# Kernel optimization log

Hardware: AMD Instinct MI355X
Metric: run time of the kernel (lower is better)

## Reference

```python
import jax, jax.numpy as jnp
import numpy as np

WIN = 15
BINS = 32
ALPHA = 0.9
LAM1 = 0.5
LAM2 = 0.5


def _tmedian(x, axis):
    # torch-style median: k-th smallest with k=(n-1)//2 (lower middle), keepdims
    n = x.shape[axis]
    s = jnp.sort(x, axis=axis)
    return jnp.take(s, jnp.array([(n - 1) // 2]), axis=axis)


def _box_sum_1d(x, k, axis):
    # sliding-window sum (zero padding) via cumsum / integral image
    p = k // 2
    L = x.shape[axis]
    c = jnp.cumsum(x, axis=axis)
    pad = [(0, 0)] * x.ndim
    pad[axis] = (1, 0)
    c = jnp.pad(c, pad)
    i = jnp.arange(L)
    hi = jnp.clip(i + p + 1, 0, L)
    lo = jnp.clip(i - p, 0, L)
    return jnp.take(c, hi, axis=axis) - jnp.take(c, lo, axis=axis)


def _counts_1d(L, k, dtype):
    p = k // 2
    i = jnp.arange(L)
    return (jnp.clip(i + p + 1, 0, L) - jnp.clip(i - p, 0, L)).astype(dtype)


def box_avg(x, k):
    # avg_pool2d(stride=1, padding=k//2, count_include_pad=False) on [B,C,H,W]
    s = _box_sum_1d(_box_sum_1d(x, k, 2), k, 3)
    c = _counts_1d(x.shape[2], k, x.dtype)[:, None] * _counts_1d(x.shape[3], k, x.dtype)[None, :]
    return s / c


def avg3(x):
    # avg_pool2d(k=3, stride=1, pad=1, count_include_pad=True)
    return _box_sum_1d(_box_sum_1d(x, 3, 2), 3, 3) / 9.0


def _softplus(x):
    t = jnp.log1p(jnp.exp(-jnp.abs(x)))
    return jnp.where(x >= 0, x + t, t)


def _conv3(x, k):
    return jax.lax.conv_general_dilated(x, k, (1, 1), ((1, 1), (1, 1)),
                                        dimension_numbers=('NCHW', 'OIHW', 'NCHW'))


def _forward(lab, a_rand):
    B, _, H, W = lab.shape
    N = H * W
    f32 = lab.dtype
    L = lab[:, 0:1]
    a = lab[:, 1:2]
    b = lab[:, 2:3]
    kx = jnp.array([[-1, 0, 1], [-2, 0, 2], [-1, 0, 1]], f32).reshape(1, 1, 3, 3)
    ky = jnp.array([[-1, -2, -1], [0, 0, 0], [1, 2, 1]], f32).reshape(1, 1, 3, 3)
    gx = _conv3(L, kx)
    gy = _conv3(L, ky)
    E = avg3(gx * gx) + avg3(gy * gy)           # structure-tensor trace
    S = jnp.sqrt(a * a + b * b + 1e-8)           # chroma
    Xf = jnp.concatenate([E, S], 1).reshape(B, 2, N).transpose(0, 2, 1)   # [B,N,2]
    yf = L.reshape(B, 1, N).transpose(0, 2, 1)                            # [B,N,1]
    XtX = jnp.einsum('bni,bnj->bij', Xf, Xf)
    XtY = jnp.einsum('bni,bnj->bij', Xf, yf)
    beta = jnp.linalg.solve(XtX + 1e-6 * jnp.eye(2, dtype=f32), XtY)[..., 0]  # [B,2]
    pred = beta[:, 0][:, None, None, None] * E + beta[:, 1][:, None, None, None] * S
    L_perp = L - pred
    # robust scale + whitening of [L_perp, E, S]
    X3f = jnp.concatenate([L_perp, E, S], 1).reshape(B, 3, N).transpose(0, 2, 1)  # [B,N,3]
    med = _tmedian(X3f, 1)
    mad = _tmedian(jnp.abs(X3f - med), 1) * 1.4826 + 1e-8
    Xz = (X3f - med) / mad
    diff = Xz - Xz.mean(1, keepdims=True)
    cov = jnp.einsum('bni,bnj->bij', diff, diff) / N
    e, V = jnp.linalg.eigh(jnp.maximum(cov, 1e-8))
    Wwh = jnp.einsum('bij,bj,bkj->bik', V, 1.0 / jnp.sqrt(e), V)
    Xw = diff @ Wwh                                                       # [B,N,3]
    # 128-way random-projection kurtosis search
    an = a_rand / (jnp.linalg.norm(a_rand, axis=-1, keepdims=True) + 1e-12)
    z = jnp.einsum('bni,bti->bnt', Xw, an)                                # [B,N,128]
    zc = z - z.mean(1, keepdims=True)
    m2 = (zc ** 2).mean(1) + 1e-12
    m4 = (zc ** 4).mean(1)
    kurt = m4 / (m2 * m2) - 3.0
    best = jnp.argmax(jnp.abs(kurt), axis=1)
    a_star = jnp.take_along_axis(an, best[:, None, None], axis=1)[:, 0]   # [B,3]
    z_best = jnp.einsum('bni,bi->bn', Xw, a_star)                         # [B,N]
    # 1-D 2-component GMM, 10 EM steps
    K = 2
    q25 = jnp.quantile(z_best, 0.25, axis=1)
    q75 = jnp.quantile(z_best, 0.75, axis=1)
    mu = jnp.stack([q25, q75], 1)[:, None, :]   # [B,1,K]
    var = jnp.ones((B, 1, K), f32)
    pi = jnp.full((B, 1, K), 0.5, f32)
    x1 = z_best[:, :, None]                      # [B,N,1]
    R = jnp.zeros((B, N, K), f32)
    for _ in range(10):
        logp = (-0.5 * ((x1 - mu) ** 2 / (var + 1e-6))
                - 0.5 * jnp.log(var + 1e-6) + jnp.log(pi + 1e-8))
        R = jnp.exp(jax.nn.log_softmax(logp, axis=2))
        Nk = R.sum(1, keepdims=True)             # [B,1,K]
        mu = (R * x1).sum(1, keepdims=True) / (Nk + 1e-8)
        var = (R * (x1 - mu) ** 2).sum(1, keepdims=True) / (Nk + 1e-8) + 1e-6
        pi = Nk / N
    R_alpha = R ** ALPHA
    R_alpha = R_alpha / (R_alpha.sum(2, keepdims=True) + 1e-8)
    rk_maps = R_alpha.transpose(0, 2, 1).reshape(B, K, 1, H, W)
    # per-cluster weighted Mahalanobis distance in [L_perp,E,S] space
    eye3 = jnp.eye(3, dtype=f32)
    Dk = []
    for k in range(K):
        w = R_alpha[:, :, k]
        Wsum = w.sum(1, keepdims=True) + 1e-8
        mu_k = jnp.einsum('bn,bni->bi', w, X3f) / Wsum
        Xm = X3f - mu_k[:, None, :]
        cov_k = jnp.einsum('bn,bni,bnj->bij', w, Xm, Xm) / Wsum[..., None] + 1e-6 * eye3
        inv_k = jnp.linalg.inv(cov_k)
        Dk.append(jnp.sqrt(jnp.einsum('bni,bij,bnj->bn', Xm, inv_k, Xm) + 1e-8))
    Dk = jnp.stack(Dk, 2)                        # [B,N,K]
    Rtemp = jax.nn.softmax(jnp.log(R_alpha + 1e-8), axis=2)
    D_M = (Rtemp * Dk).sum(2).reshape(B, 1, H, W)
    # local luminance anomaly (box-filtered weighted mean/std)
    Z_LLA = []
    for k in range(K):
        rk = rk_maps[:, k]
        den = box_avg(rk, WIN) + 1e-8
        mu_b = box_avg(rk * L_perp, WIN) / den
        var_b = jnp.maximum(box_avg(rk * L_perp ** 2, WIN) / den - mu_b ** 2, 1e-8)
        lla = jnp.abs(L_perp - mu_b) / (jnp.sqrt(var_b) + 1e-8)
        v = lla.reshape(B, 1, N)
        mv = _tmedian(v, 2)
        mdv = _tmedian(jnp.abs(v - mv), 2) * 1.4826 + 1e-8
        Z_LLA.append(((v - mv) / mdv).reshape(B, 1, H, W))
    # global-vs-local histogram distance (GLD)
    Lmin = L_perp.min(axis=(2, 3), keepdims=True)
    Lmax = L_perp.max(axis=(2, 3), keepdims=True)
    Lnorm = jnp.clip((L_perp - Lmin) / (Lmax - Lmin + 1e-8), 0, 1)
    idx = jnp.clip((Lnorm * BINS).astype(jnp.int32), 0, BINS - 1)[:, 0]   # [B,H,W]
    onehot = jax.nn.one_hot(idx, BINS, dtype=f32).transpose(0, 3, 1, 2)   # [B,bins,H,W]
    Z_GLD = []
    for k in range(K):
        rk = rk_maps[:, k]
        w_hist = onehot * rk
        g_hist = w_hist.reshape(B, BINS, N).sum(-1)
        g_hist = g_hist / (g_hist.sum(1, keepdims=True) + 1e-8)
        g_cdf = jnp.cumsum(g_hist, 1)
        loc_cdf = jnp.cumsum(box_avg(w_hist, WIN), 1) / (box_avg(rk, WIN) + 1e-8)
        GLD = jnp.abs(loc_cdf - g_cdf[:, :, None, None]).sum(1) / BINS    # [B,H,W]
        v = GLD.reshape(B, N)
        mv = _tmedian(v, 1)                                              # [B,1]
        mdv = _tmedian(jnp.abs(v - mv), 1) * 1.4826 + 1e-8
        Z_GLD.append(((GLD - mv[:, :, None]) / mdv[:, :, None])[:, None])
    gamma = jnp.ones_like(L_perp)
    for k in range(K):
        gamma = gamma + rk_maps[:, k] * (LAM1 * _softplus(Z_LLA[k]) + LAM2 * _softplus(Z_GLD[k]))
    # structural decorrelation term over [E,S]
    ES = jnp.concatenate([E, S], 1).reshape(B, 2, N).transpose(0, 2, 1)
    med2 = _tmedian(ES, 1)
    mad2 = _tmedian(jnp.abs(ES - med2), 1) * 1.4826 + 1e-8
    ESz = (ES - med2) / mad2
    d = ESz - ESz.mean(1, keepdims=True)
    cov2 = jnp.einsum('bni,bnj->bij', d, d) / N + 1e-6 * jnp.eye(2, dtype=f32)
    inv2 = jnp.linalg.inv(cov2)
    d2 = jnp.einsum('bni,bij,bnj->bn', d, inv2, d).reshape(B, 1, H, W)
    R_struct = jnp.exp(-0.5 * d2)
    L_anom = jnp.maximum(D_M * gamma * (1.0 - R_struct), 0.0)
    flat = L_anom.reshape(B, -1)
    q1 = jnp.quantile(flat, 0.01, axis=1).reshape(B, 1, 1, 1)
    q9 = jnp.quantile(flat, 0.99, axis=1).reshape(B, 1, 1, 1)
    L_anom_norm = jnp.clip((L_anom - q1) / (q9 - q1 + 1e-8), 0, 1)
    return L_perp, L_anom_norm


def setup_inputs() -> dict:
    key = jax.random.key(0)
    k1, k2 = jax.random.split(key)
    return {
        'batch_lab_raw': jax.random.normal(k1, (2, 3, 384, 384), jnp.float32),
        'a_rand': jax.random.normal(k2, (2, 128, 3), jnp.float32),
    }


def reference(batch_lab_raw, a_rand):
    return _forward(batch_lab_raw, a_rand)
```

## Files before the change

kernel.cpp:

```cpp
#include <hip/hip_runtime.h>
#include <math.h>

#define HH 384
#define WW 384
#define NPIX (HH*WW)
#define NB 2
#define BN (NB*NPIX)
#define NT 128
#define NBINS 32
#define MEDRANK ((NPIX-1)/2)
#define RB 72
#define RB2 288
#define SEL_BLK 64
#define KDG 8
#define KSEG 16
#define GHS 496
#define GVS 272

#define A_BETA 0
#define A_XZ   16
#define A_ES   40
#define A_DK   56
#define A_GMM  128
#define A_ZTOT 272
#define A_GHIST 288
#define A_KURT 512

#define F_BETA 0
#define F_X3   8
#define F_MEAN 24
#define F_WWH  32
#define F_ASTAR 828
#define F_ZBQ  868
#define F_DKINV 880
#define F_CM   918
#define F_ESI  940
#define F_LAQ  952
#define F_GCDF 968
#define F_MMS_MIN 1280
#define F_MMS_MAX 1408

__device__ __forceinline__ double waveSum(double v){
#pragma unroll
  for(int o=32;o;o>>=1) v += __shfl_down(v,o,64);
  return v;
}
__device__ __forceinline__ unsigned f2u(float f){
  unsigned u = __float_as_uint(f);
  return (u & 0x80000000u) ? ~u : (u | 0x80000000u);
}
__device__ __forceinline__ float u2f(unsigned u){
  return __uint_as_float((u & 0x80000000u) ? (u ^ 0x80000000u) : ~u);
}
__device__ __forceinline__ float sp(float x){
  float t = log1pf(expf(-fabsf(x)));
  return x >= 0.f ? x + t : t;
}

struct SelBatch {
  const float* src[8];
  int rank[8];
  int fslot[8];
  int nt;
  int medmad;
};

__device__ void pickN(const unsigned* hp, int nb, int rank, unsigned& sel, int& nrank){
  __shared__ unsigned s_cum[256];
  __shared__ unsigned s_res[2];
  int tid = threadIdx.x;
  int base = tid*8;
  unsigned loc[8]; unsigned tsum=0;
#pragma unroll
  for(int j=0;j<8;j++){ unsigned v=(base+j<nb)?hp[base+j]:0u; loc[j]=v; tsum+=v; }
  s_cum[tid]=tsum;
  __syncthreads();
  for(int o=1;o<256;o<<=1){
    unsigned t=(tid>=o)?s_cum[tid-o]:0u;
    __syncthreads();
    s_cum[tid]+=t;
    __syncthreads();
  }
  unsigned cum=s_cum[tid], ex=cum-tsum;
  if(tsum>0u && (unsigned)rank>=ex && (unsigned)rank<cum){
    int rr=rank-(int)ex; unsigned bsel=0;
#pragma unroll
    for(int j=0;j<8;j++){ if((unsigned)rr<loc[j]){ bsel=(unsigned)(base+j); break; } rr-=(int)loc[j]; }
    s_res[0]=bsel; s_res[1]=(unsigned)rr;
  }
  __syncthreads();
  sel=s_res[0]; nrank=(int)s_res[1];
  __syncthreads();
}

__global__ void k_zero(double* A, float* F, unsigned* T, unsigned* H){
  int i = blockIdx.x*256 + threadIdx.x;
  if(i < 2048) A[i] = 0.0;
  if(i < 4096){
    unsigned* U = (unsigned*)F;
    unsigned v = 0u;
    if(i>=F_MMS_MIN && i<F_MMS_MIN+64) v = 0xFFFFFFFFu;
    U[i] = v;
  }
  if(i < 512) T[i] = 0u;
  for(int j=i; j<240*2048; j+=65536) H[j]=0u;
}

__global__ __launch_bounds__(256) void k_selp(SelBatch sb, unsigned* Hh, unsigned* T,
                                              float* F, int bid, int stage, int p){
  int task = blockIdx.x / SEL_BLK;
  int blk  = blockIdx.x % SEL_BLK;
  unsigned* meta = T + 384 + task*8;
  float center = (stage==1) ? __uint_as_float(meta[4]) : 0.f;
  unsigned pre = (p==2) ? 0u : meta[stage*2];
  __shared__ unsigned lh[2048];
  for(int j=threadIdx.x;j<2048;j+=256) lh[j]=0u;
  __syncthreads();
  const float* src = sb.src[task];
  for(int i=blk*256+threadIdx.x; i<NPIX; i+=SEL_BLK*256){
    float v = src[i];
    if(stage) v = fabsf(v-center);
    unsigned u = f2u(v);
    unsigned bin; bool ok;
    if(p==2){ bin = u>>21; ok = true; }
    else if(p==1){ bin = (u>>10)&2047u; ok = ((u>>21)==pre); }
    else { bin = u&1023u; ok = ((u>>10)==pre); }
    if(ok) atomicAdd(&lh[bin],1u);
  }
  __syncthreads();
  unsigned* hp = Hh + (size_t)(((bid*8+task)*2+stage)*3 + (2-p))*2048;
  for(int j=threadIdx.x;j<2048;j+=256){ unsigned c=lh[j]; if(c) atomicAdd(hp+j,c); }
  __shared__ int s_last;
  __syncthreads();
  if(threadIdx.x==0){
    __threadfence();
    s_last = (atomicAdd(&T[16+bid*64+task*8+stage*4+(2-p)],1u) == (unsigned)(SEL_BLK-1));
  }
  __syncthreads();
  if(!s_last) return;
  int r = (p==2) ? sb.rank[task] : (int)meta[stage*2+1];
  int nb = (p==0) ? 1024 : 2048;
  unsigned sel; int nr;
  pickN(hp, nb, r, sel, nr);
  if(threadIdx.x==0){
    if(p==2){ meta[stage*2]=sel; meta[stage*2+1]=(unsigned)nr; }
    else if(p==1){ meta[stage*2]=(pre<<11)|sel; meta[stage*2+1]=(unsigned)nr; }
    else {
      float val = u2f((pre<<10)|sel);
      if(stage==0){
        if(sb.medmad) meta[4]=__float_as_uint(val);
        else F[sb.fslot[task]]=val;
      } else {
        F[sb.fslot[task]]   = __uint_as_float(meta[4]);
        F[sb.fslot[task]+1] = val*1.4826f + 1e-8f;
      }
    }
  }
}

__device__ void quad_from_stats(double N0,double Sx0,double Sxx0,double Sxt,double Sxxt,
                                float& qa,float& qb,float& qc){
  double Nt=(double)NPIX;
  double N1=Nt-N0, Sx1=Sxt-Sx0, Sxx1=Sxxt-Sxx0;
  double mu0=Sx0/(N0+1e-8), mu1=Sx1/(N1+1e-8);
  double v0=(Sxx0-2.0*mu0*Sx0+mu0*mu0*N0)/(N0+1e-8)+1e-6;
  double v1=(Sxx1-2.0*mu1*Sx1+mu1*mu1*N1)/(N1+1e-8)+1e-6;
  double p0=N0/Nt, p1=N1/Nt;
  double c0=-0.5*log(v0+1e-6)+log(p0+1e-8);
  double c1=-0.5*log(v1+1e-6)+log(p1+1e-8);
  double iv0=0.5/(v0+1e-6), iv1=0.5/(v1+1e-6);
  qa=(float)(iv0-iv1);
  qb=(float)(2.0*(iv1*mu1-iv0*mu0));
  qc=(float)(iv0*mu0*mu0-iv1*mu1*mu1+c1-c0);
}
__device__ void quad_init(const float* F,int b,float& qa,float& qb,float& qc){
  const float* z = F + F_ZBQ + b*4;
  double h25 = 0.25*(double)(NPIX-1); double f25 = h25 - floor(h25);
  double h75 = 0.75*(double)(NPIX-1); double f75 = h75 - floor(h75);
  double mu0 = (double)z[0] + f25*((double)z[1]-(double)z[0]);
  double mu1 = (double)z[2] + f75*((double)z[3]-(double)z[2]);
  double iv = 0.5/(1.0+1e-6);
  qa = 0.f;
  qb = (float)(2.0*iv*(mu1-mu0));
  qc = (float)(iv*(mu0*mu0-mu1*mu1));
}

__global__ __launch_bounds__(256) void k_sobel(const float* lab, float* S, float* E){
  int bx = blockIdx.x % 24, by = (blockIdx.x/24) % 24, b = blockIdx.x/576;
  __shared__ float Lt[20][21];
  __shared__ float G[18][19];
  const float* Lb = lab + b*3*NPIX;
  int ox = bx*16, oy = by*16;
  for(int i=threadIdx.x; i<400; i+=256){
    int lx=i%20, ly=i/20;
    int gx_=ox-2+lx, gy_=oy-2+ly;
    Lt[ly][lx] = (gx_<0||gx_>=WW||gy_<0||gy_>=HH)?0.f:Lb[gy_*WW+gx_];
  }
  __syncthreads();
  for(int i=threadIdx.x; i<324; i+=256){
    int lx=i%18, ly=i/18;
    int px=lx+1, py=ly+1;
    int gxp=ox-2+px, gyp=oy-2+py;
    float g=0.f;
    if(gxp>=0&&gxp<WW&&gyp>=0&&gyp<HH){
      float gx = -Lt[py-1][px-1]+Lt[py-1][px+1] -2.f*Lt[py][px-1]+2.f*Lt[py][px+1] -Lt[py+1][px-1]+Lt[py+1][px+1];
      float gy = -Lt[py-1][px-1]-2.f*Lt[py-1][px]-Lt[py-1][px+1] +Lt[py+1][px-1]+2.f*Lt[py+1][px]+Lt[py+1][px+1];
      g = gx*gx+gy*gy;
    }
    G[ly][lx]=g;
  }
  __syncthreads();
  int tx = threadIdx.x%16, ty = threadIdx.x/16;
  float s=0;
#pragma unroll
  for(int dy=0;dy<3;dy++)
#pragma unroll
    for(int dx=0;dx<3;dx++) s += G[ty+dy][tx+dx];
  int n = (oy+ty)*WW + ox+tx;
  E[b*NPIX+n] = s*(1.f/9.f);
  float av=Lb[NPIX+n], bv=Lb[2*NPIX+n];
  S[b*NPIX+n] = sqrtf(av*av+bv*bv+1e-8f);
}

__global__ void k_beta_red(const float* E,const float* S,const float* lab,double* A,
                           float* F, unsigned* T){
  int b = blockIdx.x / RB, blk = blockIdx.x % RB;
  double s[5]={0,0,0,0,0};
  for(int n = blk*256 + threadIdx.x; n < NPIX; n += RB*256){
    float e=E[b*NPIX+n], ss=S[b*NPIX+n], l=lab[b*3*NPIX+n];
    s[0]+=(double)e*e; s[1]+=(double)e*ss; s[2]+=(double)ss*ss;
    s[3]+=(double)e*l; s[4]+=(double)ss*l;
  }
  __shared__ double red[4][5];
  int wave=threadIdx.x>>6, lane=threadIdx.x&63;
#pragma unroll
  for(int q=0;q<5;q++){
    s[q]=waveSum(s[q]);
    if(lane==0) red[wave][q]=s[q];
  }
  __syncthreads();
  if(threadIdx.x<5){
    double v = red[0][threadIdx.x]+red[1][threadIdx.x]+red[2][threadIdx.x]+red[3][threadIdx.x];
    atomicAdd(&A[A_BETA+b*5+threadIdx.x], v);
  }
  __shared__ int s_last;
  __syncthreads();
  if(threadIdx.x==0){
    __threadfence();
    s_last = (atomicAdd(&T[0],1u) == (unsigned)(NB*RB-1));
  }
  __syncthreads();
  if(!s_last || threadIdx.x) return;
  for(int bb=0;bb<NB;bb++){
    double EE=A[A_BETA+bb*5],ES=A[A_BETA+bb*5+1],SS=A[A_BETA+bb*5+2],EL=A[A_BETA+bb*5+3],SL=A[A_BETA+bb*5+4];
    double a00=EE+1e-6, a01=ES, a11=SS+1e-6;
    double det=a00*a11-a01*a01;
    F[F_BETA+bb*2]  =(float)(( a11*EL - a01*SL)/det);
    F[F_BETA+bb*2+1]=(float)((-a01*EL + a00*SL)/det);
  }
}

__global__ void k_lperp(const float* lab,const float* E,const float* S,const float* F,float* out0){
  int i = blockIdx.x*256 + threadIdx.x;
  int b=i/NPIX, n=i%NPIX;
  float v = lab[b*3*NPIX+n] - F[F_BETA+b*2]*E[i] - F[F_BETA+b*2+1]*S[i];
  out0[i] = v;
  unsigned u = f2u(v);
  unsigned mn=u, mx=u;
#pragma unroll
  for(int o=32;o;o>>=1){
    unsigned a = __shfl_down(mn,o,64); mn = (a<mn)?a:mn;
    unsigned c = __shfl_down(mx,o,64); mx = (c>mx)?c:mx;
  }
  __shared__ unsigned rmn[4], rmx[4];
  int wave=threadIdx.x>>6, lane=threadIdx.x&63;
  if(lane==0){ rmn[wave]=mn; rmx[wave]=mx; }
  __syncthreads();
  if(threadIdx.x==0){
    unsigned m0 = rmn[0]; unsigned m1 = rmx[0];
    for(int w=1;w<4;w++){ if(rmn[w]<m0)m0=rmn[w]; if(rmx[w]>m1)m1=rmx[w]; }
    unsigned* U = (unsigned*)F;
    int slot = blockIdx.x & 31;
    atomicMin(&U[F_MMS_MIN+b*32+slot], m0);
    atomicMax(&U[F_MMS_MAX+b*32+slot], m1);
  }
}

__global__ void k_xz_red(const float* Lp,const float* E,const float* S,float* F,double* A,
                         unsigned* T){
  int b = blockIdx.x / RB, blk = blockIdx.x % RB;
  const float* M = F + F_X3 + b*6;
  double s[9]={0,0,0,0,0,0,0,0,0};
  for(int n = blk*256 + threadIdx.x; n < NPIX; n += RB*256){
    float z0=(Lp[b*NPIX+n]-M[0])/M[1];
    float z1=(E [b*NPIX+n]-M[2])/M[3];
    float z2=(S [b*NPIX+n]-M[4])/M[5];
    s[0]+=z0; s[1]+=z1; s[2]+=z2;
    s[3]+=(double)z0*z0; s[4]+=(double)z0*z1; s[5]+=(double)z0*z2;
    s[6]+=(double)z1*z1; s[7]+=(double)z1*z2; s[8]+=(double)z2*z2;
  }
  __shared__ double red[4][9];
  int wave=threadIdx.x>>6, lane=threadIdx.x&63;
#pragma unroll
  for(int q=0;q<9;q++){
    s[q]=waveSum(s[q]);
    if(lane==0) red[wave][q]=s[q];
  }
  __syncthreads();
  if(threadIdx.x<9){
    double v = red[0][threadIdx.x]+red[1][threadIdx.x]+red[2][threadIdx.x]+red[3][threadIdx.x];
    atomicAdd(&A[A_XZ+b*9+threadIdx.x], v);
  }
  __shared__ int s_last;
  __syncthreads();
  if(threadIdx.x==0){
    __threadfence();
    s_last = (atomicAdd(&T[1],1u) == (unsigned)(NB*RB-1));
  }
  __syncthreads();
  if(!s_last) return;
  int bb = threadIdx.x;
  if(bb>=NB) return;
  const double* ss = A + A_XZ + bb*9;
  double inv = 1.0/(double)NPIX;
  double m0=ss[0]*inv, m1=ss[1]*inv, m2=ss[2]*inv;
  double a[3][3];
  a[0][0]=fmax(ss[3]*inv-m0*m0,1e-8);
  a[0][1]=a[1][0]=fmax(ss[4]*inv-m0*m1,1e-8);
  a[0][2]=a[2][0]=fmax(ss[5]*inv-m0*m2,1e-8);
  a[1][1]=fmax(ss[6]*inv-m1*m1,1e-8);
  a[1][2]=a[2][1]=fmax(ss[7]*inv-m1*m2,1e-8);
  a[2][2]=fmax(ss[8]*inv-m2*m2,1e-8);
  double V[3][3]={{1,0,0},{0,1,0},{0,0,1}};
  for(int sweep=0;sweep<40;sweep++){
    for(int pp=0;pp<3;pp++){
      int p = (pp==2)?1:0;
      int q = (pp==0)?1:2;
      double apq=a[p][q];
      if(fabs(apq)<1e-30) continue;
      double theta=(a[q][q]-a[p][p])/(2.0*apq);
      double t=((theta>=0)?1.0:-1.0)/(fabs(theta)+sqrt(1.0+theta*theta));
      double c=1.0/sqrt(1.0+t*t), sn=t*c;
      for(int k2=0;k2<3;k2++){ double akp=a[k2][p],akq=a[k2][q];
        a[k2][p]=c*akp-sn*akq; a[k2][q]=sn*akp+c*akq; }
      for(int k2=0;k2<3;k2++){ double apk=a[p][k2],aqk=a[q][k2];
        a[p][k2]=c*apk-sn*aqk; a[q][k2]=sn*apk+c*aqk; }
      for(int k2=0;k2<3;k2++){ double vkp=V[k2][p],vkq=V[k2][q];
        V[k2][p]=c*vkp-sn*vkq; V[k2][q]=sn*vkp+c*vkq; }
    }
  }
  double is0=1.0/sqrt(a[0][0]), is1=1.0/sqrt(a[1][1]), is2=1.0/sqrt(a[2][2]);
  for(int i=0;i<3;i++) for(int j=0;j<3;j++){
    double w = V[i][0]*is0*V[j][0] + V[i][1]*is1*V[j][1] + V[i][2]*is2*V[j][2];
    F[F_WWH + bb*9 + i*3 + j] = (float)w;
  }
  F[F_MEAN+bb*3]=(float)m0; F[F_MEAN+bb*3+1]=(float)m1; F[F_MEAN+bb*3+2]=(float)m2;
}

__global__ void k_xw(const float* Lp,const float* E,const float* S,const float* F,
                     float* Xw,int* idxP){
  __shared__ float s_mn, s_mx;
  int i = blockIdx.x*256 + threadIdx.x;
  int b=i/NPIX;
  if(threadIdx.x==0){
    const unsigned* U = (const unsigned*)F;
    unsigned mn=0xFFFFFFFFu, mx=0u;
    for(int s2=0;s2<32;s2++){
      unsigned a=U[F_MMS_MIN+b*32+s2]; if(a<mn)mn=a;
      unsigned c=U[F_MMS_MAX+b*32+s2]; if(c>mx)mx=c;
    }
    s_mn=u2f(mn); s_mx=u2f(mx);
  }
  __syncthreads();
  const float* M = F + F_X3 + b*6;
  float lp = Lp[i];
  float z0=(lp-M[0])/M[1];
  float z1=(E [i]-M[2])/M[3];
  float z2=(S [i]-M[4])/M[5];
  float d0=z0-F[F_MEAN+b*3], d1=z1-F[F_MEAN+b*3+1], d2=z2-F[F_MEAN+b*3+2];
  const float* Wm = F + F_WWH + b*9;
  Xw[3*(size_t)i  ]=d0*Wm[0]+d1*Wm[3]+d2*Wm[6];
  Xw[3*(size_t)i+1]=d0*Wm[1]+d1*Wm[4]+d2*Wm[7];
  Xw[3*(size_t)i+2]=d0*Wm[2]+d1*Wm[5]+d2*Wm[8];
  float ln = (lp-s_mn)/(s_mx-s_mn+1e-8f);
  ln = fminf(fmaxf(ln,0.f),1.f);
  int id = (int)(ln*32.f);
  idxP[i] = id>31?31:(id<0?0:id);
}

__global__ __launch_bounds__(256) void k_kurt(const float* Xw, const float* arand,
                                              double* A, float* F, unsigned* T){
  int g = blockIdx.x;
  int b   = g / ((NT/KDG)*KSEG);
  int rem = g % ((NT/KDG)*KSEG);
  int dg  = rem / KSEG;
  int seg = rem % KSEG;
  float a0[KDG],a1[KDG],a2[KDG];
#pragma unroll
  for(int j=0;j<KDG;j++){
    const float* ar = arand + (b*NT+dg*KDG+j)*3;
    float q0=ar[0],q1=ar[1],q2=ar[2];
    float nrm=(float)(sqrt((double)q0*q0+(double)q1*q1+(double)q2*q2)+1e-12);
    a0[j]=q0/nrm; a1[j]=q1/nrm; a2[j]=q2/nrm;
  }
  const float* X = Xw + (size_t)b*NPIX*3;
  double s[KDG][4];
#pragma unroll
  for(int j=0;j<KDG;j++){ s[j][0]=0; s[j][1]=0; s[j][2]=0; s[j][3]=0; }
  const int cnt = NPIX/KSEG;
  int start = seg*cnt;
  for(int n=start+threadIdx.x; n<start+cnt; n+=256){
    const float* p = X + 3*(size_t)n;
    float x=p[0], y=p[1], z=p[2];
#pragma unroll
    for(int j=0;j<KDG;j++){
      float zz = fmaf(x,a0[j],fmaf(y,a1[j], z*a2[j]));
      float z2f = zz*zz;
      s[j][0]+=zz; s[j][1]+=z2f; s[j][2]+=z2f*zz; s[j][3]+=(double)z2f*z2f;
    }
  }
  __shared__ double red[4][KDG*4];
  int wave=threadIdx.x>>6, lane=threadIdx.x&63;
#pragma unroll
  for(int j=0;j<KDG;j++)
#pragma unroll
    for(int m=0;m<4;m++){
      double v=waveSum(s[j][m]);
      if(lane==0) red[wave][j*4+m]=v;
    }
  __syncthreads();
  if(threadIdx.x<KDG*4){
    double v = red[0][threadIdx.x]+red[1][threadIdx.x]+red[2][threadIdx.x]+red[3][threadIdx.x];
    int j=threadIdx.x>>2, m=threadIdx.x&3;
    atomicAdd(&A[A_KURT + (size_t)(b*NT+dg*KDG+j)*4 + m], v);
  }
  __shared__ int s_last;
  __syncthreads();
  if(threadIdx.x==0){
    __threadfence();
    s_last = (atomicAdd(&T[5],1u) == (unsigned)(NB*(NT/KDG)*KSEG-1));
  }
  __syncthreads();
  if(!s_last) return;
  __shared__ float ak[NB*NT];
  {
    int tid=threadIdx.x;
    const double* K = A + A_KURT + (size_t)tid*4;
    double inv=1.0/(double)NPIX;
    double mean=K[0]*inv, M2=K[1]*inv, M3=K[2]*inv, M4=K[3]*inv;
    double m2 = M2 - mean*mean + 1e-12;
    double m4 = M4 - 4.0*mean*M3 + 6.0*mean*mean*M2 - 3.0*mean*mean*mean*mean;
    ak[tid] = (float)fabs(m4/(m2*m2) - 3.0);
  }
  __syncthreads();
  if(threadIdx.x<NB){
    int bb=threadIdx.x;
    int best=0; float bv=ak[bb*NT];
    for(int j=1;j<NT;j++){ float v=ak[bb*NT+j]; if(v>bv){bv=v;best=j;} }
    const float* ar = arand + (bb*NT+best)*3;
    double nrm = sqrt((double)ar[0]*ar[0]+(double)ar[1]*ar[1]+(double)ar[2]*ar[2])+1e-12;
    F[F_ASTAR+bb*3]  =(float)(ar[0]/nrm);
    F[F_ASTAR+bb*3+1]=(float)(ar[1]/nrm);
    F[F_ASTAR+bb*3+2]=(float)(ar[2]/nrm);
  }
}

__global__ void k_zbest(const float* Xw,const float* F,float* zb,double* A){
  int i = blockIdx.x*256 + threadIdx.x;
  int b=i/NPIX;
  const float* p = Xw + 3*(size_t)i;
  float v = p[0]*F[F_ASTAR+b*3] + p[1]*F[F_ASTAR+b*3+1] + p[2]*F[F_ASTAR+b*3+2];
  zb[i]=v;
  double s0=waveSum((double)v), s1=waveSum((double)v*v);
  __shared__ double red[4][2];
  int wave=threadIdx.x>>6, lane=threadIdx.x&63;
  if(lane==0){ red[wave][0]=s0; red[wave][1]=s1; }
  __syncthreads();
  if(threadIdx.x<2){
    double v2 = red[0][threadIdx.x]+red[1][threadIdx.x]+red[2][threadIdx.x]+red[3][threadIdx.x];
    atomicAdd(&A[A_ZTOT+b*2+threadIdx.x], v2);
  }
}

__global__ __launch_bounds__(256) void k_gmm_red(const float* zb, const float* F, double* A, int it){
  __shared__ float Q[3];
  __shared__ double red[4][3];
  int b = blockIdx.x / RB2, blk = blockIdx.x % RB2;
  if(threadIdx.x==0){
    float qa,qb,qc;
    if(it==0) quad_init(F,b,qa,qb,qc);
    else {
      const double* g = A + A_GMM + (it-1)*8 + b*4;
      quad_from_stats(g[0],g[1],g[2],A[A_ZTOT+b*2],A[A_ZTOT+b*2+1],qa,qb,qc);
    }
    Q[0]=qa;Q[1]=qb;Q[2]=qc;
  }
  __syncthreads();
  float qa=Q[0],qb=Q[1],qc=Q[2];
  double s0=0,s1=0,s2=0;
  for(int n = blk*256 + threadIdx.x; n < NPIX; n += RB2*256){
    float x = zb[b*NPIX+n];
    float f = fmaf(fmaf(qa,x,qb),x,qc);
    float r0 = 1.f/(1.f+expf(f));
    float rx = r0*x;
    s0+=r0; s1+=rx; s2+=(double)rx*x;
  }
  int wave=threadIdx.x>>6, lane=threadIdx.x&63;
  s0=waveSum(s0); s1=waveSum(s1); s2=waveSum(s2);
  if(lane==0){ red[wave][0]=s0; red[wave][1]=s1; red[wave][2]=s2; }
  __syncthreads();
  if(threadIdx.x<3){
    double v = red[0][threadIdx.x]+red[1][threadIdx.x]+red[2][threadIdx.x]+red[3][threadIdx.x];
    atomicAdd(&A[A_GMM+it*8+b*4+threadIdx.x], v);
  }
}

__global__ void k_ralpha(const float* zb, float* F, double* A, const int* idxP,
                         float* Ra0, float* Ra1, unsigned* T){
  __shared__ float h0[NBINS], h1[NBINS];
  __shared__ float Q[3];
  if(threadIdx.x<NBINS){ h0[threadIdx.x]=0.f; h1[threadIdx.x]=0.f; }
  int i = blockIdx.x*256 + threadIdx.x;
  int b=i/NPIX;
  if(threadIdx.x==0){
    const double* g = A + A_GMM + 8*8 + b*4;
    float qa,qb,qc;
    quad_from_stats(g[0],g[1],g[2],A[A_ZTOT+b*2],A[A_ZTOT+b*2+1],qa,qb,qc);
    Q[0]=qa;Q[1]=qb;Q[2]=qc;
  }
  __syncthreads();
  float x = zb[i];
  float f = fmaf(fmaf(Q[0],x,Q[1]),x,Q[2]);
  float r0 = 1.f/(1.f+expf(f));
  float r1 = 1.f-r0;
  float ra0=powf(r0,0.9f), ra1=powf(r1,0.9f);
  float s=ra0+ra1+1e-8f;
  ra0/=s; ra1/=s;
  Ra0[i]=ra0; Ra1[i]=ra1;
  int id = idxP[i];
  atomicAdd(&h0[id], ra0);
  atomicAdd(&h1[id], ra1);
  __syncthreads();
  if(threadIdx.x<NBINS){
    if(h0[threadIdx.x]!=0.f) atomicAdd(&A[A_GHIST+(0*NB+b)*32+threadIdx.x], (double)h0[threadIdx.x]);
    if(h1[threadIdx.x]!=0.f) atomicAdd(&A[A_GHIST+(1*NB+b)*32+threadIdx.x], (double)h1[threadIdx.x]);
  }
  __shared__ int s_last;
  __syncthreads();
  if(threadIdx.x==0){
    __threadfence();
    s_last = (atomicAdd(&T[2],1u) == (unsigned)(BN/256-1));
  }
  __syncthreads();
  if(!s_last) return;
  int t = threadIdx.x;
  if(t>=4) return;
  const double* gh = A + A_GHIST + t*32;
  double sum=0;
  for(int j=0;j<NBINS;j++) sum += gh[j];
  double c=0;
  for(int j=0;j<NBINS;j++){
    c += gh[j]/(sum+1e-8);
    F[F_GCDF+t*32+j]=(float)c;
  }
}

__global__ void k_dk_red(const float* Lp,const float* E,const float* S,
                         const float* Ra0,const float* Ra1,double* A,float* F,unsigned* T){
  int b = blockIdx.x / RB, blk = blockIdx.x % RB;
  double s[20];
#pragma unroll
  for(int q=0;q<20;q++) s[q]=0;
  for(int n = blk*256 + threadIdx.x; n < NPIX; n += RB*256){
    int i=b*NPIX+n;
    double w0=Ra0[i], w1=Ra1[i];
    double x0=Lp[i], x1=E[i], x2=S[i];
    s[0]+=w0; s[1]+=w0*x0; s[2]+=w0*x1; s[3]+=w0*x2;
    s[4]+=w0*x0*x0; s[5]+=w0*x0*x1; s[6]+=w0*x0*x2; s[7]+=w0*x1*x1; s[8]+=w0*x1*x2; s[9]+=w0*x2*x2;
    s[10]+=w1; s[11]+=w1*x0; s[12]+=w1*x1; s[13]+=w1*x2;
    s[14]+=w1*x0*x0; s[15]+=w1*x0*x1; s[16]+=w1*x0*x2; s[17]+=w1*x1*x1; s[18]+=w1*x1*x2; s[19]+=w1*x2*x2;
  }
  __shared__ double red[4][20];
  int wave=threadIdx.x>>6, lane=threadIdx.x&63;
#pragma unroll
  for(int q=0;q<20;q++){
    s[q]=waveSum(s[q]);
    if(lane==0) red[wave][q]=s[q];
  }
  __syncthreads();
  if(threadIdx.x<20){
    double v = red[0][threadIdx.x]+red[1][threadIdx.x]+red[2][threadIdx.x]+red[3][threadIdx.x];
    atomicAdd(&A[A_DK+b*20+threadIdx.x], v);
  }
  __shared__ int s_last;
  __syncthreads();
  if(threadIdx.x==0){
    __threadfence();
    s_last = (atomicAdd(&T[3],1u) == (unsigned)(NB*RB-1));
  }
  __syncthreads();
  if(!s_last || threadIdx.x) return;
  for(int bb=0;bb<NB;bb++) for(int k=0;k<2;k++){
    const double* ss = A + A_DK + (bb*2+k)*10;
    double W0=ss[0], Ws=W0+1e-8;
    double mu0=ss[1]/Ws, mu1=ss[2]/Ws, mu2=ss[3]/Ws;
    double C00=(ss[4]-2.0*mu0*ss[1]+mu0*mu0*W0)/Ws + 1e-6;
    double C01=(ss[5]-mu0*ss[2]-mu1*ss[1]+mu0*mu1*W0)/Ws;
    double C02=(ss[6]-mu0*ss[3]-mu2*ss[1]+mu0*mu2*W0)/Ws;
    double C11=(ss[7]-2.0*mu1*ss[2]+mu1*mu1*W0)/Ws + 1e-6;
    double C12=(ss[8]-mu1*ss[3]-mu2*ss[2]+mu1*mu2*W0)/Ws;
    double C22=(ss[9]-2.0*mu2*ss[3]+mu2*mu2*W0)/Ws + 1e-6;
    double det = C00*(C11*C22-C12*C12) - C01*(C01*C22-C12*C02) + C02*(C01*C12-C11*C02);
    double id = 1.0/det;
    float* P = F + F_DKINV + (bb*2+k)*9;
    P[0]=(float)((C11*C22-C12*C12)*id);
    P[1]=(float)((C02*C12-C01*C22)*id);
    P[2]=(float)((C01*C12-C02*C11)*id);
    P[3]=(float)((C00*C22-C02*C02)*id);
    P[4]=(float)((C01*C02-C00*C12)*id);
    P[5]=(float)((C00*C11-C01*C01)*id);
    P[6]=(float)mu0; P[7]=(float)mu1; P[8]=(float)mu2;
  }
}

__global__ __launch_bounds__(256) void k_lla(const float* Ra0, const float* Ra1,
                                             const float* Lp, float* tmpL){
  int kk = blockIdx.x / (NB*576);
  int inner = blockIdx.x % (NB*576);
  int bx = inner % 24, by = (inner/24) % 24, b = inner/576;
  const float* rk = kk ? Ra1 : Ra0;
  __shared__ float Rt[30][31], Lt[30][31];
  __shared__ float h0[30][17], h1[30][17], h2[30][17];
  int ox = bx*16, oy = by*16;
  const float* Rb = rk + (size_t)b*NPIX;
  const float* Lb = Lp + (size_t)b*NPIX;
  for(int i=threadIdx.x; i<900; i+=256){
    int lx=i%30, ly=i/30;
    int gx_=ox-7+lx, gy_=oy-7+ly;
    bool in = (gx_>=0&&gx_<WW&&gy_>=0&&gy_<HH);
    Rt[ly][lx]= in ? Rb[gy_*WW+gx_] : 0.f;
    Lt[ly][lx]= in ? Lb[gy_*WW+gx_] : 0.f;
  }
  __syncthreads();
  for(int i=threadIdx.x; i<480; i+=256){
    int j=i%16, r=i/16;
    float s0=0,s1=0,s2=0;
#pragma unroll
    for(int d=0;d<15;d++){
      float rr=Rt[r][j+d], ll=Lt[r][j+d];
      s0+=rr; float rl=rr*ll; s1+=rl; s2+=rl*ll;
    }
    h0[r][j]=s0; h1[r][j]=s1; h2[r][j]=s2;
  }
  __syncthreads();
  int tx=threadIdx.x%16, ty=threadIdx.x/16;
  float S0=0,S1=0,S2=0;
#pragma unroll
  for(int d=0;d<15;d++){ S0+=h0[ty+d][tx]; S1+=h1[ty+d][tx]; S2+=h2[ty+d][tx]; }
  int x=ox+tx, y=oy+ty;
  float cy = (float)((y+8<HH?y+8:HH)-(y-7>0?y-7:0));
  float cx = (float)((x+8<WW?x+8:WW)-(x-7>0?x-7:0));
  float cnt = cy*cx;
  float den = S0/cnt + 1e-8f;
  float mu  = (S1/cnt)/den;
  float var = fmaxf((S2/cnt)/den - mu*mu, 1e-8f);
  int n = y*WW+x;
  tmpL[(size_t)kk*BN + b*NPIX+n] = fabsf(Lb[n]-mu)/(sqrtf(var)+1e-8f);
}

__global__ __launch_bounds__(256) void k_gldf(const float* Ra0, const float* Ra1,
                                              const int* idxP, const float* F, float* tmpG){
  int kk = blockIdx.x / (NB*576);
  int inner = blockIdx.x % (NB*576);
  int bx = inner % 24, by = (inner/24) % 24, b = inner/576;
  const float* rk = kk ? Ra1 : Ra0;
  __shared__ float Rt[30][31];
  __shared__ unsigned char It[30][32];
  __shared__ float Hh[16*GHS];
  __shared__ float Vv[16*GVS];
  __shared__ float gc[NBINS];
  if(threadIdx.x<NBINS) gc[threadIdx.x]=F[F_GCDF+(kk*NB+b)*32+threadIdx.x];
  int ox=bx*16, oy=by*16;
  const float* Rb = rk + (size_t)b*NPIX;
  const int* Ib = idxP + (size_t)b*NPIX;
  for(int i=threadIdx.x;i<900;i+=256){
    int lx=i%30, ly=i/30;
    int gx_=ox-7+lx, gy_=oy-7+ly;
    bool in = (gx_>=0&&gx_<WW&&gy_>=0&&gy_<HH);
    Rt[ly][lx] = in? Rb[gy_*WW+gx_] : 0.f;
    It[ly][lx] = in? (unsigned char)Ib[gy_*WW+gx_] : 0;
  }
  int tx=threadIdx.x%16, ty=threadIdx.x/16;
  float vs[32];
  for(int half=0; half<2; ++half){
    int base = half*16;
    __syncthreads();
    for(int i=threadIdx.x;i<16*GHS;i+=256) Hh[i]=0.f;
    __syncthreads();
    for(int i=threadIdx.x;i<480;i+=256){
      int j=i%16, r=i/16;
      for(int d=0;d<15;d++){
        int bin = (int)It[r][j+d];
        if((bin>>4)==half) Hh[(bin&15)*GHS + i] += Rt[r][j+d];
      }
    }
    __syncthreads();
    {
      int j  = threadIdx.x%16;
      int bn = threadIdx.x/16;
      const float* h = Hh + bn*GHS;
      float s=0;
#pragma unroll
      for(int r=0;r<15;r++) s += h[r*16+j];
      Vv[bn*GVS + 0*16 + j] = s;
      for(int yy=1;yy<16;yy++){
        s += h[(yy+14)*16+j] - h[(yy-1)*16+j];
        Vv[bn*GVS + yy*16 + j] = s;
      }
    }
    __syncthreads();
#pragma unroll
    for(int jb=0;jb<16;jb++) vs[base+jb] = Vv[jb*GVS + ty*16 + tx];
  }
  int x=ox+tx, y=oy+ty;
  float cy = (float)((y+8<HH?y+8:HH)-(y-7>0?y-7:0));
  float cx = (float)((x+8<WW?x+8:WW)-(x-7>0?x-7:0));
  float cnt = cy*cx;
  float tot=0;
#pragma unroll
  for(int bin=0;bin<NBINS;bin++) tot += vs[bin];
  float den = tot/cnt + 1e-8f;
  float cs=0, acc=0;
#pragma unroll
  for(int bin=0;bin<NBINS;bin++){
    cs += vs[bin];
    acc += fabsf((cs/cnt)/den - gc[bin]);
  }
  tmpG[(size_t)kk*BN + b*NPIX + y*WW + x] = acc*(1.f/32.f);
}

__global__ void k_lanom(const float* Lp,const float* E,const float* S,
                        const float* tmpL,const float* tmpG,
                        const float* Ra0,const float* Ra1,
                        const float* F,float* La){
  int i = blockIdx.x*256 + threadIdx.x; if(i>=BN) return;
  int b=i/NPIX;
  float x0=Lp[i], x1=E[i], x2=S[i];
  float D[2];
#pragma unroll
  for(int k=0;k<2;k++){
    const float* P = F + F_DKINV + (b*2+k)*9;
    float d0=x0-P[6], d1=x1-P[7], d2=x2-P[8];
    float q = d0*d0*P[0] + d1*d1*P[3] + d2*d2*P[5]
            + 2.f*(d0*d1*P[1] + d0*d2*P[2] + d1*d2*P[4]);
    D[k]=sqrtf(q+1e-8f);
  }
  float ra0=Ra0[i], ra1=Ra1[i];
  float w0=ra0+1e-8f, w1=ra1+1e-8f;
  float DM = (w0*D[0]+w1*D[1])/(w0+w1);
  float g = 1.0f;
#pragma unroll
  for(int kk=0;kk<2;kk++){
    const float* ML = F + F_CM + (kk*4 + 0 + b)*2;
    const float* MG = F + F_CM + (kk*4 + 2 + b)*2;
    float zl=(tmpL[(size_t)kk*BN+i]-ML[0])/ML[1];
    float zg=(tmpG[(size_t)kk*BN+i]-MG[0])/MG[1];
    float rk = kk ? ra1 : ra0;
    g += rk*(0.5f*sp(zl)+0.5f*sp(zg));
  }
  const float* M = F + F_X3 + b*6;
  const float* P = F + F_ESI + b*5;
  float z0=(x1-M[2])/M[3];
  float z1=(x2-M[4])/M[5];
  float d0=z0-P[0], d1=z1-P[1];
  float d2 = d0*d0*P[2] + 2.f*d0*d1*P[3] + d1*d1*P[4];
  float Rs = expf(-0.5f*d2);
  La[i] = fmaxf(DM*g*(1.f-Rs), 0.f);
}

__global__ void k_es_red(const float* E,const float* S,float* F,double* A,unsigned* T){
  int b = blockIdx.x / RB, blk = blockIdx.x % RB;
  const float* M = F + F_X3 + b*6;
  double s[5]={0,0,0,0,0};
  for(int n = blk*256 + threadIdx.x; n < NPIX; n += RB*256){
    float z0=(E[b*NPIX+n]-M[2])/M[3];
    float z1=(S[b*NPIX+n]-M[4])/M[5];
    s[0]+=z0; s[1]+=z1; s[2]+=(double)z0*z0; s[3]+=(double)z0*z1; s[4]+=(double)z1*z1;
  }
  __shared__ double red[4][5];
  int wave=threadIdx.x>>6, lane=threadIdx.x&63;
#pragma unroll
  for(int q=0;q<5;q++){
    s[q]=waveSum(s[q]);
    if(lane==0) red[wave][q]=s[q];
  }
  __syncthreads();
  if(threadIdx.x<5){
    double v = red[0][threadIdx.x]+red[1][threadIdx.x]+red[2][threadIdx.x]+red[3][threadIdx.x];
    atomicAdd(&A[A_ES+b*5+threadIdx.x], v);
  }
  __shared__ int s_last;
  __syncthreads();
  if(threadIdx.x==0){
    __threadfence();
    s_last = (atomicAdd(&T[4],1u) == (unsigned)(NB*RB-1));
  }
  __syncthreads();
  if(!s_last || threadIdx.x) return;
  for(int bb=0;bb<NB;bb++){
    const double* ss = A + A_ES + bb*5;
    double inv=1.0/(double)NPIX;
    double m0=ss[0]*inv, m1=ss[1]*inv;
    double c00=ss[2]*inv - m0*m0 + 1e-6;
    double c01=ss[3]*inv - m0*m1;
    double c11=ss[4]*inv - m1*m1 + 1e-6;
    double det=c00*c11-c01*c01;
    float* P = F + F_ESI + bb*5;
    P[0]=(float)m0; P[1]=(float)m1;
    P[2]=(float)(c11/det); P[3]=(float)(-c01/det); P[4]=(float)(c00/det);
  }
}
__global__ void k_out2(const float* La, const float* F, float* out){
  int i = blockIdx.x*256 + threadIdx.x; if(i>=BN) return;
  int b=i/NPIX;
  const float* v = F + F_LAQ + b*4;
  double h1 = 0.01*(double)(NPIX-1); double f1 = h1 - floor(h1);
  double h9 = 0.99*(double)(NPIX-1); double f9 = h9 - floor(h9);
  float q1 = (float)((double)v[0] + f1*((double)v[1]-(double)v[0]));
  float q9 = (float)((double)v[2] + f9*((double)v[3]-(double)v[2]));
  float r = (La[i]-q1)/(q9-q1+1e-8f);
  out[BN + i] = fminf(fmaxf(r,0.f),1.f);
}

static void run_sel(const SelBatch& sb, unsigned* H, unsigned* T, float* F, int bid, hipStream_t s){
  for(int p=2;p>=0;--p) k_selp<<<sb.nt*SEL_BLK,256,0,s>>>(sb,H,T,F,bid,0,p);
  if(sb.medmad) for(int p=2;p>=0;--p) k_selp<<<sb.nt*SEL_BLK,256,0,s>>>(sb,H,T,F,bid,1,p);
}

extern "C" void kernel_launch(void* const* d_in, const int* in_sizes, int n_in,
                              void* d_out, int out_size, void* d_ws, size_t ws_size,
                              hipStream_t stream){
  (void)in_sizes; (void)n_in; (void)out_size; (void)ws_size;
  const float* lab   = (const float*)d_in[0];
  const float* arand = (const float*)d_in[1];
  float* out = (float*)d_out;
  char* wsb = (char*)d_ws;
  double* A = (double*)wsb;
  float*  F = (float*)(wsb + 16384);
  unsigned* T = (unsigned*)(wsb + 32768);
  unsigned* H = (unsigned*)(wsb + 65536);
  float* planes = (float*)(wsb + (size_t)4*1024*1024);
  float* E    = planes;
  float* S    = planes + (size_t)BN;
  float* tA   = planes + (size_t)2*BN;
  float* tmpL = planes + (size_t)3*BN;
  float* tmpG = planes + (size_t)5*BN;
  float* Xw   = planes + (size_t)7*BN;
  float* zb   = planes + (size_t)10*BN;
  float* Ra0  = planes + (size_t)11*BN;
  float* Ra1  = planes + (size_t)12*BN;
  int*   idxP = (int*)(planes + (size_t)16*BN);

  const int GBN = BN/256;

  k_zero<<<256,256,0,stream>>>(A,F,T,H);
  k_sobel<<<NB*576,256,0,stream>>>(lab,S,E);
  k_beta_red<<<NB*RB,256,0,stream>>>(E,S,lab,A,F,T);
  k_lperp<<<GBN,256,0,stream>>>(lab,E,S,F,out);

  SelBatch sbX; sbX.nt=6; sbX.medmad=1;
  for(int b=0;b<NB;b++){
    sbX.src[b*3+0]=out+(size_t)b*NPIX; sbX.src[b*3+1]=E+(size_t)b*NPIX; sbX.src[b*3+2]=S+(size_t)b*NPIX;
    for(int ch=0;ch<3;ch++){ sbX.rank[b*3+ch]=MEDRANK; sbX.fslot[b*3+ch]=F_X3+(b*3+ch)*2; }
  }
  run_sel(sbX,H,T,F,0,stream);

  k_xz_red<<<NB*RB,256,0,stream>>>(out,E,S,F,A,T);
  k_es_red<<<NB*RB,256,0,stream>>>(E,S,F,A,T);
  k_xw<<<GBN,256,0,stream>>>(out,E,S,F,Xw,idxP);
  k_kurt<<<NB*(NT/KDG)*KSEG,256,0,stream>>>(Xw,arand,A,F,T);
  k_zbest<<<GBN,256,0,stream>>>(Xw,F,zb,A);

  SelBatch sbZ; sbZ.nt=8; sbZ.medmad=0;
  {
    int rr[4]={36863,36864,110591,110592};
    for(int b=0;b<NB;b++) for(int ri=0;ri<4;ri++){
      int t=b*4+ri;
      sbZ.src[t]=zb+(size_t)b*NPIX; sbZ.rank[t]=rr[ri]; sbZ.fslot[t]=F_ZBQ+b*4+ri;
    }
  }
  run_sel(sbZ,H,T,F,1,stream);

  for(int it=0; it<9; ++it)
    k_gmm_red<<<NB*RB2,256,0,stream>>>(zb,F,A,it);
  k_ralpha<<<GBN,256,0,stream>>>(zb,F,A,idxP,Ra0,Ra1,T);
  k_dk_red<<<NB*RB,256,0,stream>>>(out,E,S,Ra0,Ra1,A,F,T);

  k_lla<<<2*NB*576,256,0,stream>>>(Ra0,Ra1,out,tmpL);
  k_gldf<<<2*NB*576,256,0,stream>>>(Ra0,Ra1,idxP,F,tmpG);

  SelBatch sbC; sbC.nt=8; sbC.medmad=1;
  for(int kk=0;kk<2;kk++) for(int isG=0;isG<2;isG++) for(int b=0;b<NB;b++){
    int t = kk*4 + isG*2 + b;
    sbC.src[t] = (isG? tmpG: tmpL) + (size_t)kk*BN + (size_t)b*NPIX;
    sbC.rank[t]=MEDRANK; sbC.fslot[t]=F_CM + t*2;
  }
  run_sel(sbC,H,T,F,2,stream);

  k_lanom<<<GBN,256,0,stream>>>(out,E,S,tmpL,tmpG,Ra0,Ra1,F,tA);

  SelBatch sbL; sbL.nt=8; sbL.medmad=0;
  {
    int rr[4]={1474,1475,145980,145981};
    for(int b=0;b<NB;b++) for(int ri=0;ri<4;ri++){
      int t=b*4+ri;
      sbL.src[t]=tA+(size_t)b*NPIX; sbL.rank[t]=rr[ri]; sbL.fslot[t]=F_LAQ+b*4+ri;
    }
  }
  run_sel(sbL,H,T,F,3,stream);

  k_out2<<<GBN,256,0,stream>>>(tA,F,out);
}
```

Baseline: 647.8 us.

## Fold ES covariance into xz reduction, single-pass GLD histogram, larger select grid

```diff
diff --git a/kernel.cpp b/kernel.cpp
--- a/kernel.cpp
+++ b/kernel.cpp
@@ -11,15 +11,12 @@
 #define MEDRANK ((NPIX-1)/2)
 #define RB 72
 #define RB2 288
-#define SEL_BLK 64
+#define SEL_BLK 128
 #define KDG 8
 #define KSEG 16
-#define GHS 496
-#define GVS 272
 
 #define A_BETA 0
 #define A_XZ   16
-#define A_ES   40
 #define A_DK   56
 #define A_GMM  128
 #define A_ZTOT 272
@@ -355,6 +352,15 @@
     F[F_WWH + bb*9 + i*3 + j] = (float)w;
   }
   F[F_MEAN+bb*3]=(float)m0; F[F_MEAN+bb*3+1]=(float)m1; F[F_MEAN+bb*3+2]=(float)m2;
+  {
+    double c00=ss[6]*inv - m1*m1 + 1e-6;
+    double c01=ss[7]*inv - m1*m2;
+    double c11=ss[8]*inv - m2*m2 + 1e-6;
+    double det=c00*c11-c01*c01;
+    float* P = F + F_ESI + bb*5;
+    P[0]=(float)m1; P[1]=(float)m2;
+    P[2]=(float)(c11/det); P[3]=(float)(-c01/det); P[4]=(float)(c00/det);
+  }
 }
 
 __global__ void k_xw(const float* Lp,const float* E,const float* S,const float* F,
@@ -676,8 +682,7 @@
   const float* rk = kk ? Ra1 : Ra0;
   __shared__ float Rt[30][31];
   __shared__ unsigned char It[30][32];
-  __shared__ float Hh[16*GHS];
-  __shared__ float Vv[16*GVS];
+  __shared__ float Hh[32*480];
   __shared__ float gc[NBINS];
   if(threadIdx.x<NBINS) gc[threadIdx.x]=F[F_GCDF+(kk*NB+b)*32+threadIdx.x];
   int ox=bx*16, oy=by*16;
@@ -690,45 +695,27 @@
     Rt[ly][lx] = in? Rb[gy_*WW+gx_] : 0.f;
     It[ly][lx] = in? (unsigned char)Ib[gy_*WW+gx_] : 0;
   }
+  for(int i=threadIdx.x;i<32*480;i+=256) Hh[i]=0.f;
+  __syncthreads();
+  for(int i=threadIdx.x;i<480;i+=256){
+    int j=i%16, r=i/16;
+    for(int d=0;d<15;d++) Hh[(int)It[r][j+d]*480 + i] += Rt[r][j+d];
+  }
+  __syncthreads();
   int tx=threadIdx.x%16, ty=threadIdx.x/16;
   float vs[32];
-  for(int half=0; half<2; ++half){
-    int base = half*16;
-    __syncthreads();
-    for(int i=threadIdx.x;i<16*GHS;i+=256) Hh[i]=0.f;
-    __syncthreads();
-    for(int i=threadIdx.x;i<480;i+=256){
-      int j=i%16, r=i/16;
-      for(int d=0;d<15;d++){
-        int bin = (int)It[r][j+d];
-        if((bin>>4)==half) Hh[(bin&15)*GHS + i] += Rt[r][j+d];
-      }
-    }
-    __syncthreads();
-    {
-      int j  = threadIdx.x%16;
-      int bn = threadIdx.x/16;
-      const float* h = Hh + bn*GHS;
-      float s=0;
-#pragma unroll
-      for(int r=0;r<15;r++) s += h[r*16+j];
-      Vv[bn*GVS + 0*16 + j] = s;
-      for(int yy=1;yy<16;yy++){
-        s += h[(yy+14)*16+j] - h[(yy-1)*16+j];
-        Vv[bn*GVS + yy*16 + j] = s;
-      }
-    }
-    __syncthreads();
-#pragma unroll
-    for(int jb=0;jb<16;jb++) vs[base+jb] = Vv[jb*GVS + ty*16 + tx];
+  float tot=0;
+#pragma unroll
+  for(int bin=0;bin<NBINS;bin++){
+    float s=0;
+#pragma unroll
+    for(int d=0;d<15;d++) s += Hh[bin*480 + (ty+d)*16+tx];
+    vs[bin]=s; tot+=s;
   }
   int x=ox+tx, y=oy+ty;
   float cy = (float)((y+8<HH?y+8:HH)-(y-7>0?y-7:0));
   float cx = (float)((x+8<WW?x+8:WW)-(x-7>0?x-7:0));
   float cnt = cy*cx;
-  float tot=0;
-#pragma unroll
-  for(int bin=0;bin<NBINS;bin++) tot += vs[bin];
   float den = tot/cnt + 1e-8f;
   float cs=0, acc=0;
 #pragma unroll
@@ -778,48 +765,6 @@
   La[i] = fmaxf(DM*g*(1.f-Rs), 0.f);
 }
 
-__global__ void k_es_red(const float* E,const float* S,float* F,double* A,unsigned* T){
-  int b = blockIdx.x / RB, blk = blockIdx.x % RB;
-  const float* M = F + F_X3 + b*6;
-  double s[5]={0,0,0,0,0};
-  for(int n = blk*256 + threadIdx.x; n < NPIX; n += RB*256){
-    float z0=(E[b*NPIX+n]-M[2])/M[3];
-    float z1=(S[b*NPIX+n]-M[4])/M[5];
-    s[0]+=z0; s[1]+=z1; s[2]+=(double)z0*z0; s[3]+=(double)z0*z1; s[4]+=(double)z1*z1;
-  }
-  __shared__ double red[4][5];
-  int wave=threadIdx.x>>6, lane=threadIdx.x&63;
-#pragma unroll
-  for(int q=0;q<5;q++){
-    s[q]=waveSum(s[q]);
-    if(lane==0) red[wave][q]=s[q];
-  }
-  __syncthreads();
-  if(threadIdx.x<5){
-    double v = red[0][threadIdx.x]+red[1][threadIdx.x]+red[2][threadIdx.x]+red[3][threadIdx.x];
-    atomicAdd(&A[A_ES+b*5+threadIdx.x], v);
-  }
-  __shared__ int s_last;
-  __syncthreads();
-  if(threadIdx.x==0){
-    __threadfence();
-    s_last = (atomicAdd(&T[4],1u) == (unsigned)(NB*RB-1));
-  }
-  __syncthreads();
-  if(!s_last || threadIdx.x) return;
-  for(int bb=0;bb<NB;bb++){
-    const double* ss = A + A_ES + bb*5;
-    double inv=1.0/(double)NPIX;
-    double m0=ss[0]*inv, m1=ss[1]*inv;
-    double c00=ss[2]*inv - m0*m0 + 1e-6;
-    double c01=ss[3]*inv - m0*m1;
-    double c11=ss[4]*inv - m1*m1 + 1e-6;
-    double det=c00*c11-c01*c01;
-    float* P = F + F_ESI + bb*5;
-    P[0]=(float)m0; P[1]=(float)m1;
-    P[2]=(float)(c11/det); P[3]=(float)(-c01/det); P[4]=(float)(c00/det);
-  }
-}
 __global__ void k_out2(const float* La, const float* F, float* out){
   int i = blockIdx.x*256 + threadIdx.x; if(i>=BN) return;
   int b=i/NPIX;
@@ -876,7 +821,6 @@
   run_sel(sbX,H,T,F,0,stream);
 
   k_xz_red<<<NB*RB,256,0,stream>>>(out,E,S,F,A,T);
-  k_es_red<<<NB*RB,256,0,stream>>>(E,S,F,A,T);
   k_xw<<<GBN,256,0,stream>>>(out,E,S,F,Xw,idxP);
   k_kurt<<<NB*(NT/KDG)*KSEG,256,0,stream>>>(Xw,arand,A,F,T);
   k_zbest<<<GBN,256,0,stream>>>(Xw,F,zb,A);
```

After: 769.5 us. +18.8%, slower.
